# Kernel tuning notes

Hardware: AMD Instinct MI355X
Metric: run time of the kernel (lower is better)

## Reference

```python
import jax, jax.numpy as jnp
import numpy as np

B, N, D = 2, 512, 256
H, HD = 4, 64  # hidden_dim=256 split across 4 heads (is_concat=True)
SLOPE = 0.2


def setup_inputs() -> dict:
    key = jax.random.key(0)
    ks = jax.random.split(key, 8)
    rn = lambda k, sh: jax.random.normal(k, sh, dtype=jnp.float32)
    return {
        "query": rn(ks[0], (B, N, D)),
        "key_in": rn(ks[1], (B, N, D)),
        "value": rn(ks[2], (B, N, D)),
        "w_q": rn(ks[3], (D, H * HD)) * 0.05,  # shared query/key projection (share_weights=True)
        "b_q": rn(ks[4], (H * HD,)) * 0.05,
        "w_v": rn(ks[5], (D, H * HD)) * 0.05,
        "b_v": rn(ks[6], (H * HD,)) * 0.05,
        "a": rn(ks[7], (HD,)) * 0.05,  # attention Linear(hd, 1, bias=False), shared across heads
    }


def reference(query, key_in, value, w_q, b_q, w_v, b_v, a):
    hq = (query @ w_q + b_q).reshape(B, N, H, HD)
    hk = (key_in @ w_q + b_q).reshape(B, N, H, HD)  # share_weights=True
    hv = (value @ w_v + b_v).reshape(B, N, H, HD)
    # torch repeat/repeat_interleave + view gives h[b,i,j] = hq[b,j] + hk[b,i]
    h = hq[:, None, :, :, :] + hk[:, :, None, :, :]  # [B, N, N, H, HD]
    e = jnp.einsum('bijhf,f->bijh', jax.nn.leaky_relu(h, SLOPE), a)
    e = jax.nn.softmax(e, axis=2)  # softmax over source nodes j (dropout is identity in eval)
    out = jnp.einsum('bijh,bjhf->bihf', e, hv).reshape(B, N, H * HD)  # is_concat
    h_prime = jax.nn.relu(out)
    return h_prime, e
```

## Files before the change

kernel.cpp:

```cpp
#include <hip/hip_runtime.h>


#define NB 2
#define NN 512
#define DD 256
#define NH 4
#define HDIM 64

typedef __attribute__((ext_vector_type(2))) float f32x2;

__device__ __forceinline__ float rl(float v, int u) {
    return __uint_as_float(__builtin_amdgcn_readlane(__float_as_uint(v), u));
}
__device__ __forceinline__ f32x2 pk_fma(f32x2 a, f32x2 b, f32x2 c) {
    return __builtin_elementwise_fma(a, b, c);
}
__device__ __forceinline__ f32x2 pk_abs(f32x2 t) {
    return __builtin_elementwise_max(t, -t);
}

__global__ __launch_bounds__(256, 4) void proj_kernel(
    const float* __restrict__ q, const float* __restrict__ kin, const float* __restrict__ vin,
    const float* __restrict__ wq, const float* __restrict__ bq,
    const float* __restrict__ wv, const float* __restrict__ bv,
    float* __restrict__ hq, float* __restrict__ hk, float* __restrict__ hv)
{
    const int m = blockIdx.z;
    const float* x    = (m == 0) ? q  : (m == 1) ? kin : vin;
    const float* w    = (m == 2) ? wv : wq;
    const float* bias = (m == 2) ? bv : bq;
    float* out        = (m == 0) ? hq : (m == 1) ? hk : hv;

    const int r0 = blockIdx.x * 16;
    const int cb = blockIdx.y * 128;
    const int t  = threadIdx.x;

    __shared__ float xs[16][DD + 4];

    #pragma unroll
    for (int p = 0; p < 4; ++p) {
        const int idx = t + 256 * p;
        const int row = idx >> 6;
        const int kc  = idx & 63;
        const float4 v = *reinterpret_cast<const float4*>(&x[(size_t)(r0 + row) * DD + kc * 4]);
        *reinterpret_cast<float4*>(&xs[row][kc * 4]) = v;
    }
    __syncthreads();

    const int row0 = (t >> 5) * 2;
    const int c0   = (t & 31) * 4;

    const float4 b4 = *reinterpret_cast<const float4*>(&bias[cb + c0]);
    float acc[2][4];
    #pragma unroll
    for (int r = 0; r < 2; ++r) { acc[r][0]=b4.x; acc[r][1]=b4.y; acc[r][2]=b4.z; acc[r][3]=b4.w; }

    for (int kt = 0; kt < DD; kt += 4) {
        const float4 a0 = *reinterpret_cast<const float4*>(&xs[row0][kt]);
        const float4 a1 = *reinterpret_cast<const float4*>(&xs[row0 + 1][kt]);
        const float xa0[4] = {a0.x, a0.y, a0.z, a0.w};
        const float xa1[4] = {a1.x, a1.y, a1.z, a1.w};
        #pragma unroll
        for (int kk = 0; kk < 4; ++kk) {
            const float4 w4 = *reinterpret_cast<const float4*>(&w[(size_t)(kt + kk) * DD + cb + c0]);
            const float wv4[4] = {w4.x, w4.y, w4.z, w4.w};
            #pragma unroll
            for (int c = 0; c < 4; ++c) {
                acc[0][c] = fmaf(xa0[kk], wv4[c], acc[0][c]);
                acc[1][c] = fmaf(xa1[kk], wv4[c], acc[1][c]);
            }
        }
    }
    #pragma unroll
    for (int r = 0; r < 2; ++r) {
        float4 o; o.x = acc[r][0]; o.y = acc[r][1]; o.z = acc[r][2]; o.w = acc[r][3];
        *reinterpret_cast<float4*>(&out[(size_t)(r0 + row0 + r) * DD + cb + c0]) = o;
    }
}

__global__ __launch_bounds__(256, 4) void attn_kernel(
    const float* __restrict__ hq, const float* __restrict__ hk, const float* __restrict__ hv,
    const float* __restrict__ a, float* __restrict__ out_hp, float* __restrict__ out_e)
{
    const int t   = threadIdx.x;
    const int b   = blockIdx.x >> 9;
    const int rem = blockIdx.x & 511;
    const int i0  = (rem >> 2) * 4;
    const int h   = rem & 3;

    __shared__ float s[4][NN + 8];
    __shared__ float part[4][4][HDIM];

    const float* hk0 = hk + ((size_t)(b * NN) + i0) * DD + h * HDIM;

    {
        const int j0 = t * 2;
        const float* qbase = hq + ((size_t)(b * NN) + j0) * DD + h * HDIM;
        f32x2 accu[2] = {{0.f, 0.f}, {0.f, 0.f}};
        f32x2 acc[2][4] = {};
        #pragma unroll
        for (int half = 0; half < 2; ++half) {
            float4 qb[16];
            #pragma unroll
            for (int fc = 0; fc < 8; ++fc) {
                qb[fc]     = *reinterpret_cast<const float4*>(qbase + half * 32 + fc * 4);
                qb[fc + 8] = *reinterpret_cast<const float4*>(qbase + DD + half * 32 + fc * 4);
            }
            __builtin_amdgcn_sched_barrier(0);
            #pragma unroll
            for (int fc = 0; fc < 8; ++fc) {
                const int fo = half * 32 + fc * 4;
                const float4 a4 = *reinterpret_cast<const float4*>(a + fo);
                const f32x2 av[2] = {{a4.x, a4.y}, {a4.z, a4.w}};
                f32x2 kk[4][2];
                #pragma unroll
                for (int ii = 0; ii < 4; ++ii) {
                    const float4 kv = *reinterpret_cast<const float4*>(hk0 + ii * DD + fo);
                    kk[ii][0] = f32x2{kv.x, kv.y}; kk[ii][1] = f32x2{kv.z, kv.w};
                }
                #pragma unroll
                for (int jj = 0; jj < 2; ++jj) {
                    const float4 q4 = qb[jj * 8 + fc];
                    const f32x2 qv[2] = {{q4.x, q4.y}, {q4.z, q4.w}};
                    #pragma unroll
                    for (int cp = 0; cp < 2; ++cp) {
                        accu[jj] = pk_fma(qv[cp], av[cp], accu[jj]);
                        #pragma unroll
                        for (int ii = 0; ii < 4; ++ii) {
                            const f32x2 t2 = qv[cp] + kk[ii][cp];
                            acc[jj][ii] = pk_fma(pk_abs(t2), av[cp], acc[jj][ii]);
                        }
                    }
                }
            }
        }
        #pragma unroll
        for (int jj = 0; jj < 2; ++jj) {
            const float su = 0.6f * (accu[jj].x + accu[jj].y);
            #pragma unroll
            for (int ii = 0; ii < 4; ++ii)
                s[ii][j0 + jj] = fmaf(0.4f, acc[jj][ii].x + acc[jj][ii].y, su);
        }
    }
    __syncthreads();

    {
        const int wv = t >> 6, lane = t & 63;
        float* row = &s[wv][0];
        float vals[8]; float mx = -1e30f;
        #pragma unroll
        for (int k2 = 0; k2 < 8; ++k2) { vals[k2] = row[lane + 64 * k2]; mx = fmaxf(mx, vals[k2]); }
        #pragma unroll
        for (int off = 32; off; off >>= 1) mx = fmaxf(mx, __shfl_xor(mx, off, 64));
        float sum = 0.f;
        #pragma unroll
        for (int k2 = 0; k2 < 8; ++k2) { vals[k2] = __expf(vals[k2] - mx); sum += vals[k2]; }
        #pragma unroll
        for (int off = 32; off; off >>= 1) sum += __shfl_xor(sum, off, 64);
        const float inv = 1.0f / sum;
        #pragma unroll
        for (int k2 = 0; k2 < 8; ++k2) row[lane + 64 * k2] = vals[k2] * inv;
    }
    __syncthreads();

    {
        float* oe = out_e + (((size_t)(b * NN) + i0) * NN) * NH + h;
        #pragma unroll
        for (int k2 = 0; k2 < 8; ++k2) {
            const int idx = t + 256 * k2;
            const int ii = idx >> 9;
            const int j  = idx & 511;
            oe[((size_t)ii * NN + j) * NH] = s[ii][j];
        }
    }

    {
        const int col  = t & 63;
        const int jg   = t >> 6;
        const int lane = t & 63;
        f32x2 acc2[4] = {};
        const float* hvb = hv + (size_t)(b * NN) * DD + h * HDIM + col;
        #pragma unroll
        for (int ch = 0; ch < 2; ++ch) {
            const int jbase = jg * 128 + ch * 64;
            const float e0 = s[0][jbase + lane];
            const float e1 = s[1][jbase + lane];
            const float e2 = s[2][jbase + lane];
            const float e3 = s[3][jbase + lane];
            #pragma unroll
            for (int ub = 0; ub < 4; ++ub) {
                float hvv[16];
                #pragma unroll
                for (int k = 0; k < 16; ++k)
                    hvv[k] = hvb[(size_t)(jbase + ub * 16 + k) * DD];
                __builtin_amdgcn_sched_barrier(0);
                #pragma unroll
                for (int k = 0; k < 16; k += 2) {
                    const int u = ub * 16 + k;
                    const f32x2 hv2 = {hvv[k], hvv[k + 1]};
                    acc2[0] = pk_fma(f32x2{rl(e0, u), rl(e0, u + 1)}, hv2, acc2[0]);
                    acc2[1] = pk_fma(f32x2{rl(e1, u), rl(e1, u + 1)}, hv2, acc2[1]);
                    acc2[2] = pk_fma(f32x2{rl(e2, u), rl(e2, u + 1)}, hv2, acc2[2]);
                    acc2[3] = pk_fma(f32x2{rl(e3, u), rl(e3, u + 1)}, hv2, acc2[3]);
                }
            }
        }
        #pragma unroll
        for (int ii = 0; ii < 4; ++ii) part[jg][ii][col] = acc2[ii].x + acc2[ii].y;
    }
    __syncthreads();
    {
        const int ii = t >> 6, col = t & 63;
        const float v = part[0][ii][col] + part[1][ii][col] + part[2][ii][col] + part[3][ii][col];
        out_hp[((size_t)(b * NN) + i0 + ii) * DD + h * HDIM + col] = v > 0.f ? v : 0.f;
    }
}

extern "C" void kernel_launch(void* const* d_in, const int* in_sizes, int n_in,
                              void* d_out, int out_size, void* d_ws, size_t ws_size,
                              hipStream_t stream) {
    const float* q   = (const float*)d_in[0];
    const float* kin = (const float*)d_in[1];
    const float* vin = (const float*)d_in[2];
    const float* wq  = (const float*)d_in[3];
    const float* bq  = (const float*)d_in[4];
    const float* wv  = (const float*)d_in[5];
    const float* bv  = (const float*)d_in[6];
    const float* a   = (const float*)d_in[7];

    float* out_hp = (float*)d_out;
    float* out_e  = out_hp + (size_t)NB * NN * DD;

    float* hq = (float*)d_ws;
    float* hk = hq + (size_t)NB * NN * DD;
    float* hv = hk + (size_t)NB * NN * DD;

    proj_kernel<<<dim3(64, 2, 3), 256, 0, stream>>>(q, kin, vin, wq, bq, wv, bv, hq, hk, hv);
    attn_kernel<<<dim3(NB * 128 * NH), 256, 0, stream>>>(hq, hk, hv, a, out_hp, out_e);
}
```

Measured before the change: 120.4 us.

## Process eight query rows per attention block with 512 threads

Each attention block now covers 8 target rows instead of 4 and runs 512 threads, with one source node per thread in the score phase. Every hq load and every hv load is reused across twice as many rows, and the grid is halved. The cost is more live registers per thread (8 score accumulators, 8 e values, 16 hq vectors). The launch bound of 512 threads with 4 blocks per CU tightens the register budget, so spills or lower occupancy are possible.

```diff
diff --git a/kernel.cpp b/kernel.cpp
--- a/kernel.cpp
+++ b/kernel.cpp
@@ -78,69 +78,59 @@
     }
 }
 
-__global__ __launch_bounds__(256, 4) void attn_kernel(
+__global__ __launch_bounds__(512, 4) void attn_kernel(
     const float* __restrict__ hq, const float* __restrict__ hk, const float* __restrict__ hv,
     const float* __restrict__ a, float* __restrict__ out_hp, float* __restrict__ out_e)
 {
     const int t   = threadIdx.x;
-    const int b   = blockIdx.x >> 9;
-    const int rem = blockIdx.x & 511;
-    const int i0  = (rem >> 2) * 4;
+    const int b   = blockIdx.x >> 8;
+    const int rem = blockIdx.x & 255;
+    const int i0  = (rem >> 2) * 8;
     const int h   = rem & 3;
 
-    __shared__ float s[4][NN + 8];
-    __shared__ float part[4][4][HDIM];
+    __shared__ float s[8][NN + 8];
+    __shared__ float part[8][8][HDIM];
 
     const float* hk0 = hk + ((size_t)(b * NN) + i0) * DD + h * HDIM;
 
     {
-        const int j0 = t * 2;
-        const float* qbase = hq + ((size_t)(b * NN) + j0) * DD + h * HDIM;
-        f32x2 accu[2] = {{0.f, 0.f}, {0.f, 0.f}};
-        f32x2 acc[2][4] = {};
-        #pragma unroll
-        for (int half = 0; half < 2; ++half) {
-            float4 qb[16];
-            #pragma unroll
-            for (int fc = 0; fc < 8; ++fc) {
-                qb[fc]     = *reinterpret_cast<const float4*>(qbase + half * 32 + fc * 4);
-                qb[fc + 8] = *reinterpret_cast<const float4*>(qbase + DD + half * 32 + fc * 4);
-            }
-            __builtin_amdgcn_sched_barrier(0);
-            #pragma unroll
-            for (int fc = 0; fc < 8; ++fc) {
-                const int fo = half * 32 + fc * 4;
-                const float4 a4 = *reinterpret_cast<const float4*>(a + fo);
-                const f32x2 av[2] = {{a4.x, a4.y}, {a4.z, a4.w}};
-                f32x2 kk[4][2];
+        const int j = t;
+        const float* qbase = hq + ((size_t)(b * NN) + j) * DD + h * HDIM;
+        float4 qb[16];
+        #pragma unroll
+        for (int fc = 0; fc < 16; ++fc)
+            qb[fc] = *reinterpret_cast<const float4*>(qbase + fc * 4);
+        __builtin_amdgcn_sched_barrier(0);
+
+        f32x2 accu = {0.f, 0.f};
+        f32x2 acc[8] = {};
+        #pragma unroll
+        for (int fc = 0; fc < 16; ++fc) {
+            const int fo = fc * 4;
+            const float4 a4 = *reinterpret_cast<const float4*>(a + fo);
+            const f32x2 av[2] = {{a4.x, a4.y}, {a4.z, a4.w}};
+            f32x2 kk[8][2];
+            #pragma unroll
+            for (int ii = 0; ii < 8; ++ii) {
+                const float4 kv = *reinterpret_cast<const float4*>(hk0 + ii * DD + fo);
+                kk[ii][0] = f32x2{kv.x, kv.y}; kk[ii][1] = f32x2{kv.z, kv.w};
+            }
+            const float4 q4 = qb[fc];
+            const f32x2 qv[2] = {{q4.x, q4.y}, {q4.z, q4.w}};
+            #pragma unroll
+            for (int cp = 0; cp < 2; ++cp) {
+                accu = pk_fma(qv[cp], av[cp], accu);
                 #pragma unroll
-                for (int ii = 0; ii < 4; ++ii) {
-                    const float4 kv = *reinterpret_cast<const float4*>(hk0 + ii * DD + fo);
-                    kk[ii][0] = f32x2{kv.x, kv.y}; kk[ii][1] = f32x2{kv.z, kv.w};
+                for (int ii = 0; ii < 8; ++ii) {
+                    const f32x2 t2 = qv[cp] + kk[ii][cp];
+                    acc[ii] = pk_fma(pk_abs(t2), av[cp], acc[ii]);
                 }
-                #pragma unroll
-                for (int jj = 0; jj < 2; ++jj) {
-                    const float4 q4 = qb[jj * 8 + fc];
-                    const f32x2 qv[2] = {{q4.x, q4.y}, {q4.z, q4.w}};
-                    #pragma unroll
-                    for (int cp = 0; cp < 2; ++cp) {
-                        accu[jj] = pk_fma(qv[cp], av[cp], accu[jj]);
-                        #pragma unroll
-                        for (int ii = 0; ii < 4; ++ii) {
-                            const f32x2 t2 = qv[cp] + kk[ii][cp];
-                            acc[jj][ii] = pk_fma(pk_abs(t2), av[cp], acc[jj][ii]);
-                        }
-                    }
-                }
-            }
-        }
-        #pragma unroll
-        for (int jj = 0; jj < 2; ++jj) {
-            const float su = 0.6f * (accu[jj].x + accu[jj].y);
-            #pragma unroll
-            for (int ii = 0; ii < 4; ++ii)
-                s[ii][j0 + jj] = fmaf(0.4f, acc[jj][ii].x + acc[jj][ii].y, su);
-        }
+            }
+        }
+        const float su = 0.6f * (accu.x + accu.y);
+        #pragma unroll
+        for (int ii = 0; ii < 8; ++ii)
+            s[ii][j] = fmaf(0.4f, acc[ii].x + acc[ii].y, su);
     }
     __syncthreads();
 
@@ -167,7 +157,7 @@
         float* oe = out_e + (((size_t)(b * NN) + i0) * NN) * NH + h;
         #pragma unroll
         for (int k2 = 0; k2 < 8; ++k2) {
-            const int idx = t + 256 * k2;
+            const int idx = t + 512 * k2;
             const int ii = idx >> 9;
             const int j  = idx & 511;
             oe[((size_t)ii * NN + j) * NH] = s[ii][j];
@@ -178,40 +168,37 @@
         const int col  = t & 63;
         const int jg   = t >> 6;
         const int lane = t & 63;
-        f32x2 acc2[4] = {};
+        const int jbase = jg * 64;
+        f32x2 acc2[8] = {};
         const float* hvb = hv + (size_t)(b * NN) * DD + h * HDIM + col;
-        #pragma unroll
-        for (int ch = 0; ch < 2; ++ch) {
-            const int jbase = jg * 128 + ch * 64;
-            const float e0 = s[0][jbase + lane];
-            const float e1 = s[1][jbase + lane];
-            const float e2 = s[2][jbase + lane];
-            const float e3 = s[3][jbase + lane];
-            #pragma unroll
-            for (int ub = 0; ub < 4; ++ub) {
-                float hvv[16];
+        float e[8];
+        #pragma unroll
+        for (int ii = 0; ii < 8; ++ii) e[ii] = s[ii][jbase + lane];
+        #pragma unroll
+        for (int ub = 0; ub < 4; ++ub) {
+            float hvv[16];
+            #pragma unroll
+            for (int k = 0; k < 16; ++k)
+                hvv[k] = hvb[(size_t)(jbase + ub * 16 + k) * DD];
+            __builtin_amdgcn_sched_barrier(0);
+            #pragma unroll
+            for (int k = 0; k < 16; k += 2) {
+                const int u = ub * 16 + k;
+                const f32x2 hv2 = {hvv[k], hvv[k + 1]};
                 #pragma unroll
-                for (int k = 0; k < 16; ++k)
-                    hvv[k] = hvb[(size_t)(jbase + ub * 16 + k) * DD];
-                __builtin_amdgcn_sched_barrier(0);
-                #pragma unroll
-                for (int k = 0; k < 16; k += 2) {
-                    const int u = ub * 16 + k;
-                    const f32x2 hv2 = {hvv[k], hvv[k + 1]};
-                    acc2[0] = pk_fma(f32x2{rl(e0, u), rl(e0, u + 1)}, hv2, acc2[0]);
-                    acc2[1] = pk_fma(f32x2{rl(e1, u), rl(e1, u + 1)}, hv2, acc2[1]);
-                    acc2[2] = pk_fma(f32x2{rl(e2, u), rl(e2, u + 1)}, hv2, acc2[2]);
-                    acc2[3] = pk_fma(f32x2{rl(e3, u), rl(e3, u + 1)}, hv2, acc2[3]);
-                }
-            }
-        }
-        #pragma unroll
-        for (int ii = 0; ii < 4; ++ii) part[jg][ii][col] = acc2[ii].x + acc2[ii].y;
+                for (int ii = 0; ii < 8; ++ii)
+                    acc2[ii] = pk_fma(f32x2{rl(e[ii], u), rl(e[ii], u + 1)}, hv2, acc2[ii]);
+            }
+        }
+        #pragma unroll
+        for (int ii = 0; ii < 8; ++ii) part[jg][ii][col] = acc2[ii].x + acc2[ii].y;
     }
     __syncthreads();
     {
         const int ii = t >> 6, col = t & 63;
-        const float v = part[0][ii][col] + part[1][ii][col] + part[2][ii][col] + part[3][ii][col];
+        float v = 0.f;
+        #pragma unroll
+        for (int jg = 0; jg < 8; ++jg) v += part[jg][ii][col];
         out_hp[((size_t)(b * NN) + i0 + ii) * DD + h * HDIM + col] = v > 0.f ? v : 0.f;
     }
 }
@@ -236,5 +223,5 @@
     float* hv = hk + (size_t)NB * NN * DD;
 
     proj_kernel<<<dim3(64, 2, 3), 256, 0, stream>>>(q, kin, vin, wq, bq, wv, bv, hq, hk, hv);
-    attn_kernel<<<dim3(NB * 128 * NH), 256, 0, stream>>>(hq, hk, hv, a, out_hp, out_e);
-}
+    attn_kernel<<<dim3(NB * 64 * NH), 512, 0, stream>>>(hq, hk, hv, a, out_hp, out_e);
+}
```

Result: slower. 131.1 us (+8.9%).
